# Kernel optimization log

Hardware: AMD Instinct MI355X
Metric: run time of the kernel (lower is better)

Reference implementation:

```python
import jax, jax.numpy as jnp
import numpy as np
import math

EPS = 1e-5
K = 4        # conv kernel size
N = 16       # d_state


def setup_inputs() -> dict:
    key = jax.random.key(0)
    b, l, d = 1, 2048, 1024
    di = 2 * d                      # inner channels after split
    dt_rank = math.ceil(d / 16)     # 64
    ks = jax.random.split(key, 8)
    s = 0.02
    return {
        "x": jax.random.normal(ks[0], (b, l, d), jnp.float32),
        "norm_scale": jnp.ones((d,), jnp.float32),
        "w_in": jax.random.normal(ks[1], (d, 4 * d), jnp.float32) * s,
        "conv_w": jax.random.normal(ks[2], (K, 1, di), jnp.float32) * 0.2,
        "conv_b": jnp.zeros((di,), jnp.float32),
        "A_log": jax.random.normal(ks[3], (di, N), jnp.float32) * 0.5,
        "D": jax.random.normal(ks[4], (di,), jnp.float32) * 0.1,
        "w_xproj": jax.random.normal(ks[5], (di, dt_rank + 2 * N), jnp.float32) * s,
        "w_dt": jax.random.normal(ks[6], (dt_rank, di), jnp.float32) * s,
        "b_dt": jnp.zeros((di,), jnp.float32),
        "w_out": jax.random.normal(ks[7], (di, d), jnp.float32) * s,
    }


def _causal_depthwise_conv(x, w, b):
    # x: (b,l,c), w: (K,1,c). Original pads (K-1,K-1) then slices [:, :l] == causal left-pad.
    c = x.shape[-1]
    y = jax.lax.conv_general_dilated(
        x, w, window_strides=(1,), padding=[(K - 1, 0)],
        dimension_numbers=("NWC", "WIO", "NWC"), feature_group_count=c)
    return y + b


def reference(x, norm_scale, w_in, conv_w, conv_b, A_log, D, w_xproj, w_dt, b_dt, w_out):
    dt_rank = w_dt.shape[0]
    # RMSNorm (mean=False, bias=False), scale only
    h = x * jax.lax.rsqrt(jnp.mean(x * x, axis=-1, keepdims=True) + EPS) * norm_scale
    h = h @ w_in                         # (b,l,4d)
    xs, res = jnp.split(h, 2, axis=-1)   # each (b,l,2d)
    res = jax.nn.silu(res)
    xs = jax.nn.silu(_causal_depthwise_conv(xs, conv_w, conv_b))
    proj = xs @ w_xproj                  # (b,l,dt_rank+2N)
    delta, B, C = jnp.split(proj, [dt_rank, dt_rank + N], axis=-1)
    delta = jax.nn.softplus(delta @ w_dt + b_dt)          # (b,l,c)
    A = -jnp.exp(A_log)                                   # (c,n)
    deltaA = jnp.exp(delta[..., None] * A)                # (b,l,c,n)
    deltaBx = (delta * xs)[..., None] * B[:, :, None, :]  # (b,l,c,n)

    def combine(e_i, e_j):
        a_i, b_i = e_i
        a_j, b_j = e_j
        return (a_i * a_j, a_j * b_i + b_j)

    _, ys = jax.lax.associative_scan(combine, (deltaA, deltaBx), axis=1)
    y = jnp.einsum("blcn,bln->blc", ys, C)
    out = (y + xs * D) * res
    return x + out @ w_out
```

## Files before the change

### kernel.cpp

```cpp
#include <hip/hip_runtime.h>

typedef short short8 __attribute__((ext_vector_type(8)));
typedef float floatx4 __attribute__((ext_vector_type(4)));
typedef unsigned int u32;

__device__ __forceinline__ float b2f(unsigned short u) {
    union { unsigned int i; float f; } v; v.i = ((unsigned int)u) << 16; return v.f;
}
__device__ __forceinline__ float hi2f(u32 p) {
    union { unsigned int i; float f; } v; v.i = p & 0xFFFF0000u; return v.f;
}
__device__ __forceinline__ float lo2f(u32 p) {
    union { unsigned int i; float f; } v; v.i = p << 16; return v.f;
}
__device__ __forceinline__ unsigned short f2b(float f) {
    union { unsigned int i; float f; } v; v.f = f;
    unsigned int r = v.i + 0x7FFFu + ((v.i >> 16) & 1u);
    return (unsigned short)(r >> 16);
}
__device__ __forceinline__ float ld(const void* p, size_t i, int f) {
    return f ? ((const float*)p)[i] : b2f(((const unsigned short*)p)[i]);
}
__device__ __forceinline__ int dtf(const void* scale) {
    return (((const unsigned short*)scale)[0] == 0x3F80u) ? 0 : 1;
}
__device__ __forceinline__ void gload16(const unsigned short* g, unsigned short* l) {
    __builtin_amdgcn_global_load_lds(
        (const __attribute__((address_space(1))) u32*)(const void*)g,
        (__attribute__((address_space(3))) u32*)(void*)l, 16, 0, 0);
}
template<int CTRL>
__device__ __forceinline__ float dpp_add(float y) {
    union { float f; int i; } u, r;
    u.f = y;
    r.i = __builtin_amdgcn_update_dpp(0, u.i, CTRL, 0xF, 0xF, true);
    return y + r.f;
}
#define LOG2E 1.44269504f

__global__ __launch_bounds__(256) void prep_kernel(
    const void* x, const void* scale, unsigned short* __restrict__ h,
    const void* w_in, unsigned short* __restrict__ wT,
    const void* w_out, unsigned short* __restrict__ woT)
{
    const int f = dtf(scale);
    const int b = blockIdx.x, tid = threadIdx.x;
    if (b < 2048) {
        const int t = b;
        float xv[4];
        float ss = 0.f;
        #pragma unroll
        for (int j = 0; j < 4; j++) {
            xv[j] = ld(x, (size_t)t * 1024 + j * 256 + tid, f);
            ss += xv[j] * xv[j];
        }
        #pragma unroll
        for (int o = 32; o > 0; o >>= 1) ss += __shfl_down(ss, o);
        __shared__ float sr[4];
        if ((tid & 63) == 0) sr[tid >> 6] = ss;
        __syncthreads();
        float r = rsqrtf((sr[0] + sr[1] + sr[2] + sr[3]) * (1.f / 1024.f) + 1e-5f);
        #pragma unroll
        for (int j = 0; j < 4; j++) {
            int i = j * 256 + tid;
            h[(size_t)t * 1024 + i] = f2b(xv[j] * r * ld(scale, i, f));
        }
    } else if (b < 3072) {
        __shared__ unsigned short tile[64][68];
        const int idx = b - 2048;
        const int n0 = (idx & 63) * 64, k0 = (idx >> 6) * 64;
        #pragma unroll
        for (int j = 0; j < 16; j++) {
            int ii = tid + 256 * j, r = ii >> 6, c = ii & 63;
            tile[r][c] = f2b(ld(w_in, (size_t)(k0 + r) * 4096 + n0 + c, f));
        }
        __syncthreads();
        #pragma unroll
        for (int j = 0; j < 16; j++) {
            int ii = tid + 256 * j, r = ii >> 6, c = ii & 63;
            wT[(size_t)(n0 + r) * 1024 + k0 + c] = tile[c][r];
        }
    } else {
        __shared__ unsigned short tile[64][68];
        const int idx = b - 3072;
        const int n0 = (idx & 15) * 64, k0 = (idx >> 4) * 64;
        #pragma unroll
        for (int j = 0; j < 16; j++) {
            int ii = tid + 256 * j, r = ii >> 6, c = ii & 63;
            tile[r][c] = f2b(ld(w_out, (size_t)(k0 + r) * 1024 + n0 + c, f));
        }
        __syncthreads();
        #pragma unroll
        for (int j = 0; j < 16; j++) {
            int ii = tid + 256 * j, r = ii >> 6, c = ii & 63;
            woT[(size_t)(n0 + r) * 2048 + k0 + c] = tile[c][r];
        }
    }
}

template<int KDIM, int NDIM, int TM, int MODE>
__global__ __launch_bounds__(256) void gemm_bt_kernel(
    const unsigned short* __restrict__ A, const unsigned short* __restrict__ BT,
    void* out0, unsigned short* out1, const void* xres, const void* nscale)
{
    constexpr int RT = TM / 32;
    const int f = dtf(nscale);
    __shared__ __align__(16) unsigned short As[TM * 64];
    __shared__ __align__(16) unsigned short Bs[64 * 64];
    const int t = threadIdx.x, w = t >> 6, lane = t & 63;
    const int q = lane >> 4, low = lane & 15;
    const int row0 = blockIdx.y * TM, n0 = blockIdx.x * 64;
    const int wy = w >> 1, wx = w & 1;

    floatx4 acc[RT][2];
    #pragma unroll
    for (int i = 0; i < RT; i++)
        #pragma unroll
        for (int j = 0; j < 2; j++) acc[i][j] = (floatx4){0.f, 0.f, 0.f, 0.f};

    const int srow = lane >> 3, scol = (lane & 7) * 8;
    const unsigned short* a_src = A + (size_t)(row0 + w * (TM / 4) + srow) * KDIM + scol;
    const unsigned short* b_src = BT + (size_t)(n0 + w * 16 + srow) * KDIM + scol;

    for (int k0 = 0; k0 < KDIM; k0 += 64) {
        #pragma unroll
        for (int i = 0; i < TM / 32; i++)
            gload16(a_src + k0 + i * 8 * KDIM, &As[(w * (TM / 4) + i * 8) * 64]);
        #pragma unroll
        for (int i = 0; i < 2; i++)
            gload16(b_src + k0 + i * 8 * KDIM, &Bs[(w * 16 + i * 8) * 64]);
        __syncthreads();
        #pragma unroll
        for (int kh = 0; kh < 2; kh++) {
            short8 af[RT];
            #pragma unroll
            for (int rt = 0; rt < RT; rt++)
                af[rt] = *(const short8*)&As[(wy * (TM / 2) + rt * 16 + low) * 64 + kh * 32 + q * 8];
            #pragma unroll
            for (int nt = 0; nt < 2; nt++) {
                short8 bf = *(const short8*)&Bs[(wx * 32 + nt * 16 + low) * 64 + kh * 32 + q * 8];
                #pragma unroll
                for (int rt = 0; rt < RT; rt++)
                    acc[rt][nt] = __builtin_amdgcn_mfma_f32_16x16x32_bf16(af[rt], bf, acc[rt][nt], 0, 0, 0);
            }
        }
        __syncthreads();
    }

    #pragma unroll
    for (int nt = 0; nt < 2; nt++) {
        const int col = n0 + wx * 32 + nt * 16 + low;
        #pragma unroll
        for (int rt = 0; rt < RT; rt++) {
            #pragma unroll
            for (int r = 0; r < 4; r++) {
                const int row = row0 + wy * (TM / 2) + rt * 16 + q * 4 + r;
                float v = acc[rt][nt][r];
                if (MODE == 0) {
                    if (col < NDIM / 2) {
                        ((unsigned short*)out0)[(size_t)row * (NDIM / 2) + col] = f2b(v);
                    } else {
                        float s = v / (1.f + __expf(-v));
                        out1[(size_t)row * (NDIM / 2) + (col - NDIM / 2)] = f2b(s);
                    }
                } else {
                    size_t idx = (size_t)row * NDIM + col;
                    float o = v + ld(xres, idx, f);
                    if (f) ((float*)out0)[idx] = o;
                    else   ((unsigned short*)out0)[idx] = f2b(o);
                }
            }
        }
    }
}

__global__ __launch_bounds__(256) void conv_kernel(
    const unsigned short* __restrict__ xs_raw, const void* conv_w,
    const void* conv_b, unsigned short* __restrict__ xs_conv, const void* nscale)
{
    const int f = dtf(nscale);
    int id = blockIdx.x * 256 + threadIdx.x;
    int t = id >> 8, c8 = (id & 255) * 8;
    float acc[8];
    if (f) {
        const float* bf = (const float*)conv_b + c8;
        float4 b0 = *(const float4*)bf, b1 = *(const float4*)(bf + 4);
        acc[0] = b0.x; acc[1] = b0.y; acc[2] = b0.z; acc[3] = b0.w;
        acc[4] = b1.x; acc[5] = b1.y; acc[6] = b1.z; acc[7] = b1.w;
    } else {
        uint4 bv = *(const uint4*)((const unsigned short*)conv_b + c8);
        const unsigned short* bp = (const unsigned short*)&bv;
        #pragma unroll
        for (int j = 0; j < 8; j++) acc[j] = b2f(bp[j]);
    }
    #pragma unroll
    for (int k = 0; k < 4; k++) {
        int tt = t - 3 + k;
        if (tt >= 0) {
            uint4 xv = *(const uint4*)(xs_raw + (size_t)tt * 2048 + c8);
            const unsigned short* xp = (const unsigned short*)&xv;
            float wv[8];
            if (f) {
                const float* wf = (const float*)conv_w + (size_t)k * 2048 + c8;
                float4 w0 = *(const float4*)wf, w1 = *(const float4*)(wf + 4);
                wv[0] = w0.x; wv[1] = w0.y; wv[2] = w0.z; wv[3] = w0.w;
                wv[4] = w1.x; wv[5] = w1.y; wv[6] = w1.z; wv[7] = w1.w;
            } else {
                uint4 wu = *(const uint4*)((const unsigned short*)conv_w + (size_t)k * 2048 + c8);
                const unsigned short* wp = (const unsigned short*)&wu;
                #pragma unroll
                for (int j = 0; j < 8; j++) wv[j] = b2f(wp[j]);
            }
            #pragma unroll
            for (int j = 0; j < 8; j++) acc[j] += wv[j] * b2f(xp[j]);
        }
    }
    unsigned short outv[8];
    #pragma unroll
    for (int j = 0; j < 8; j++) {
        float s = acc[j] / (1.f + __expf(-acc[j]));
        outv[j] = f2b(s);
    }
    *(uint4*)(xs_conv + (size_t)t * 2048 + c8) = *(const uint4*)outv;
}

__global__ __launch_bounds__(256) void xproj_gemm_kernel(
    const unsigned short* __restrict__ A, const void* B,
    float* __restrict__ partials, const void* nscale)
{
    const int f = dtf(nscale);
    __shared__ __align__(16) unsigned short As[64 * 32];
    __shared__ __align__(16) unsigned short Bs[64 * 32];
    const int t = threadIdx.x;
    const int row0 = blockIdx.y * 64, n0 = blockIdx.x * 64;
    const int ks = blockIdx.z;
    const int wave = t >> 6, lane = t & 63;
    const int q = lane >> 4, low = lane & 15;
    floatx4 acc[4];
    #pragma unroll
    for (int i = 0; i < 4; i++) acc[i] = (floatx4){0.f, 0.f, 0.f, 0.f};
    const int ar = t >> 2, ac = (t & 3) * 8;
    const int bk = t >> 3, bn = (t & 7) * 8;
    const int col0 = n0 + bn;
    const int kbeg = ks * 256, kend = kbeg + 256;
    for (int k0 = kbeg; k0 < kend; k0 += 32) {
        uint4 av = *(const uint4*)(A + (size_t)(row0 + ar) * 2048 + k0 + ac);
        *(uint4*)&As[ar * 32 + ac] = av;
        unsigned short bu[8];
        if (col0 < 96) {
            if (f) {
                const float* Bf = (const float*)B + (size_t)(k0 + bk) * 96 + col0;
                float4 b0 = *(const float4*)Bf, b1 = *(const float4*)(Bf + 4);
                bu[0] = f2b(b0.x); bu[1] = f2b(b0.y); bu[2] = f2b(b0.z); bu[3] = f2b(b0.w);
                bu[4] = f2b(b1.x); bu[5] = f2b(b1.y); bu[6] = f2b(b1.z); bu[7] = f2b(b1.w);
            } else {
                uint4 bv = *(const uint4*)((const unsigned short*)B + (size_t)(k0 + bk) * 96 + col0);
                *(uint4*)bu = bv;
            }
        } else {
            #pragma unroll
            for (int j = 0; j < 8; j++) bu[j] = 0;
        }
        #pragma unroll
        for (int j = 0; j < 8; j++) Bs[(bn + j) * 32 + bk] = bu[j];
        __syncthreads();
        short8 af = *(const short8*)&As[(wave * 16 + low) * 32 + q * 8];
        #pragma unroll
        for (int i = 0; i < 4; i++) {
            short8 bfr = *(const short8*)&Bs[(i * 16 + low) * 32 + q * 8];
            acc[i] = __builtin_amdgcn_mfma_f32_16x16x32_bf16(af, bfr, acc[i], 0, 0, 0);
        }
        __syncthreads();
    }
    float* out = partials + (size_t)ks * (2048 * 128);
    #pragma unroll
    for (int i = 0; i < 4; i++) {
        int col = n0 + i * 16 + low;
        #pragma unroll
        for (int r = 0; r < 4; r++) {
            int row = row0 + wave * 16 + q * 4 + r;
            out[(size_t)row * 128 + col] = acc[i][r];
        }
    }
}

__global__ __launch_bounds__(256) void xproj_reduce_kernel(
    const float* __restrict__ partials, float* __restrict__ proj)
{
    int id = blockIdx.x * 256 + threadIdx.x;
    float s = 0.f;
    #pragma unroll
    for (int k = 0; k < 8; k++) s += partials[(size_t)k * (2048 * 128) + id];
    proj[id] = s;
}

__global__ __launch_bounds__(256) void delta_gemm_kernel(
    const float* __restrict__ proj, const void* B, const void* b_dt,
    unsigned short* __restrict__ delta, const void* nscale)
{
    const int f = dtf(nscale);
    __shared__ __align__(16) unsigned short As[64 * 32];
    __shared__ __align__(16) unsigned short Bs[64 * 32];
    const int t = threadIdx.x;
    const int row0 = blockIdx.y * 64, n0 = blockIdx.x * 64;
    const int wave = t >> 6, lane = t & 63;
    const int q = lane >> 4, low = lane & 15;
    floatx4 acc[4];
    #pragma unroll
    for (int i = 0; i < 4; i++) acc[i] = (floatx4){0.f, 0.f, 0.f, 0.f};
    const int ar = t >> 2, ac = (t & 3) * 8;
    const int bk = t >> 3, bn = (t & 7) * 8;
    #pragma unroll
    for (int k0 = 0; k0 < 64; k0 += 32) {
        const float* Ap = proj + (size_t)(row0 + ar) * 128 + k0 + ac;
        float4 a0 = *(const float4*)Ap, a1 = *(const float4*)(Ap + 4);
        As[ar * 32 + ac + 0] = f2b(a0.x); As[ar * 32 + ac + 1] = f2b(a0.y);
        As[ar * 32 + ac + 2] = f2b(a0.z); As[ar * 32 + ac + 3] = f2b(a0.w);
        As[ar * 32 + ac + 4] = f2b(a1.x); As[ar * 32 + ac + 5] = f2b(a1.y);
        As[ar * 32 + ac + 6] = f2b(a1.z); As[ar * 32 + ac + 7] = f2b(a1.w);
        unsigned short bu[8];
        if (f) {
            const float* Bp = (const float*)B + (size_t)(k0 + bk) * 2048 + n0 + bn;
            float4 b0 = *(const float4*)Bp, b1 = *(const float4*)(Bp + 4);
            bu[0] = f2b(b0.x); bu[1] = f2b(b0.y); bu[2] = f2b(b0.z); bu[3] = f2b(b0.w);
            bu[4] = f2b(b1.x); bu[5] = f2b(b1.y); bu[6] = f2b(b1.z); bu[7] = f2b(b1.w);
        } else {
            uint4 bv = *(const uint4*)((const unsigned short*)B + (size_t)(k0 + bk) * 2048 + n0 + bn);
            const unsigned short* bp = (const unsigned short*)&bv;
            #pragma unroll
            for (int j = 0; j < 8; j++) bu[j] = bp[j];
        }
        #pragma unroll
        for (int j = 0; j < 8; j++) Bs[(bn + j) * 32 + bk] = bu[j];
        __syncthreads();
        short8 af = *(const short8*)&As[(wave * 16 + low) * 32 + q * 8];
        #pragma unroll
        for (int i = 0; i < 4; i++) {
            short8 bfr = *(const short8*)&Bs[(i * 16 + low) * 32 + q * 8];
            acc[i] = __builtin_amdgcn_mfma_f32_16x16x32_bf16(af, bfr, acc[i], 0, 0, 0);
        }
        __syncthreads();
    }
    #pragma unroll
    for (int i = 0; i < 4; i++) {
        int col = n0 + i * 16 + low;
        float bias = ld(b_dt, col, f);
        #pragma unroll
        for (int r = 0; r < 4; r++) {
            int row = row0 + wave * 16 + q * 4 + r;
            float v = acc[i][r] + bias;
            float sp = fmaxf(v, 0.f) + log1pf(__expf(-fabsf(v)));
            delta[(size_t)row * 2048 + col] = f2b(sp);
        }
    }
}

__global__ __launch_bounds__(256) void scanA_kernel(
    const unsigned short* __restrict__ delta, const unsigned short* __restrict__ xs,
    const float* __restrict__ proj, const void* A_log,
    float* __restrict__ Aprod, float* __restrict__ Send, const void* nscale)
{
    const int f = dtf(nscale);
    const int chunk = blockIdx.x, c0 = blockIdx.y * 16, t0 = chunk * 64;
    __shared__ __align__(16) u32 dxl[16 * 68];
    __shared__ __align__(16) float Bt[16 * 68];
    const int tid = threadIdx.x;
    #pragma unroll
    for (int j = 0; j < 2; j++) {
        int idx = tid + 256 * j;
        int t = idx >> 3, cp = (idx & 7) * 2;
        u32 dpair = *(const u32*)(delta + (size_t)(t0 + t) * 2048 + c0 + cp);
        u32 xpair = *(const u32*)(xs    + (size_t)(t0 + t) * 2048 + c0 + cp);
        dxl[cp * 68 + t]       = (dpair << 16) | (xpair & 0xFFFFu);
        dxl[(cp + 1) * 68 + t] = (dpair & 0xFFFF0000u) | (xpair >> 16);
    }
    #pragma unroll
    for (int j = 0; j < 4; j++) {
        int idx = tid + 256 * j;
        int t = idx >> 4, n = idx & 15;
        Bt[n * 68 + t] = proj[(size_t)(t0 + t) * 128 + 64 + n];
    }
    __syncthreads();
    const int cl = tid >> 4, n = tid & 15;
    const float A2 = -__expf(ld(A_log, (size_t)(c0 + cl) * 16 + n, f)) * LOG2E;
    float s = 0.f, dsum = 0.f;
    for (int t4 = 0; t4 < 64; t4 += 4) {
        uint4  dx4 = *(const uint4*)&dxl[cl * 68 + t4];
        float4 b4  = *(const float4*)&Bt[n * 68 + t4];
        const u32* dxp = (const u32*)&dx4;
        const float* bp = (const float*)&b4;
        #pragma unroll
        for (int j = 0; j < 4; j++) {
            u32 p = dxp[j];
            float dv = hi2f(p), xv = lo2f(p);
            float a = exp2f(dv * A2);
            s = a * s + dv * xv * bp[j];
            dsum += dv;
        }
    }
    size_t o = (size_t)chunk * 32768 + (size_t)c0 * 16 + tid;
    Aprod[o] = exp2f(A2 * dsum);
    Send[o]  = s;
}

__global__ __launch_bounds__(256) void scanB_kernel(
    const float* __restrict__ Aprod, const float* __restrict__ Send,
    float* __restrict__ prefix)
{
    int g = blockIdx.x * 256 + threadIdx.x;
    float a[32], b[32];
    #pragma unroll
    for (int k = 0; k < 32; k++) { a[k] = Aprod[(size_t)k * 32768 + g]; b[k] = Send[(size_t)k * 32768 + g]; }
    float s = 0.f;
    #pragma unroll
    for (int k = 0; k < 32; k++) { prefix[(size_t)k * 32768 + g] = s; s = a[k] * s + b[k]; }
}

__global__ __launch_bounds__(256) void scanC_kernel(
    const unsigned short* __restrict__ delta, const unsigned short* __restrict__ xs,
    const float* __restrict__ proj, const void* A_log, const void* Dv,
    const float* __restrict__ prefix,
    const unsigned short* __restrict__ res, unsigned short* __restrict__ inner,
    const void* nscale)
{
    const int f = dtf(nscale);
    const int chunk = blockIdx.x, c0 = blockIdx.y * 16, t0 = chunk * 64;
    __shared__ __align__(16) u32 dxl[16 * 68];
    __shared__ __align__(16) float Bt[16 * 68];
    __shared__ __align__(16) float Ct[16 * 68];
    __shared__ __align__(16) float yl[16 * 68];
    __shared__ float Dl[16];
    const int tid = threadIdx.x;
    if (tid < 16) Dl[tid] = ld(Dv, c0 + tid, f);
    float s = prefix[(size_t)chunk * 32768 + (size_t)c0 * 16 + tid];
    #pragma unroll
    for (int j = 0; j < 2; j++) {
        int idx = tid + 256 * j;
        int t = idx >> 3, cp = (idx & 7) * 2;
        u32 dpair = *(const u32*)(delta + (size_t)(t0 + t) * 2048 + c0 + cp);
        u32 xpair = *(const u32*)(xs    + (size_t)(t0 + t) * 2048 + c0 + cp);
        dxl[cp * 68 + t]       = (dpair << 16) | (xpair & 0xFFFFu);
        dxl[(cp + 1) * 68 + t] = (dpair & 0xFFFF0000u) | (xpair >> 16);
    }
    #pragma unroll
    for (int j = 0; j < 4; j++) {
        int idx = tid + 256 * j;
        int t = idx >> 4, n = idx & 15;
        Bt[n * 68 + t] = proj[(size_t)(t0 + t) * 128 + 64 + n];
        Ct[n * 68 + t] = proj[(size_t)(t0 + t) * 128 + 80 + n];
    }
    __syncthreads();
    const int cl = tid >> 4, n = tid & 15;
    const float A2 = -__expf(ld(A_log, (size_t)(c0 + cl) * 16 + n, f)) * LOG2E;
    for (int t4 = 0; t4 < 64; t4 += 4) {
        uint4  dx4 = *(const uint4*)&dxl[cl * 68 + t4];
        float4 b4  = *(const float4*)&Bt[n * 68 + t4];
        float4 c4  = *(const float4*)&Ct[n * 68 + t4];
        const u32* dxp = (const u32*)&dx4;
        const float* bp = (const float*)&b4;
        const float* cp = (const float*)&c4;
        #pragma unroll
        for (int j = 0; j < 4; j++) {
            u32 p = dxp[j];
            float dv = hi2f(p), xv = lo2f(p);
            float a = exp2f(dv * A2);
            s = a * s + dv * xv * bp[j];
            float y = s * cp[j];
            y = dpp_add<0x111>(y);
            y = dpp_add<0x112>(y);
            y = dpp_add<0x114>(y);
            y = dpp_add<0x118>(y);
            if (n == 15) yl[cl * 68 + t4 + j] = y;
        }
    }
    __syncthreads();
    const int et = tid >> 2, ech = (tid & 3) * 4;
    size_t gbase = (size_t)(t0 + et) * 2048 + c0 + ech;
    uint2 rv2 = *(const uint2*)(res + gbase);
    const unsigned short* rp = (const unsigned short*)&rv2;
    unsigned short outv[4];
    #pragma unroll
    for (int j = 0; j < 4; j++) {
        int c = ech + j;
        float y  = yl[c * 68 + et];
        float xv = lo2f(dxl[c * 68 + et]);
        float o  = (y + xv * Dl[c]) * b2f(rp[j]);
        outv[j] = f2b(o);
    }
    *(uint2*)(inner + gbase) = *(const uint2*)outv;
}

extern "C" void kernel_launch(void* const* d_in, const int* in_sizes, int n_in,
                              void* d_out, int out_size, void* d_ws, size_t ws_size,
                              hipStream_t stream) {
    const void* x       = d_in[0];
    const void* nscale  = d_in[1];
    const void* w_in    = d_in[2];
    const void* conv_w  = d_in[3];
    const void* conv_b  = d_in[4];
    const void* A_log   = d_in[5];
    const void* Dv      = d_in[6];
    const void* w_xproj = d_in[7];
    const void* w_dt    = d_in[8];
    const void* b_dt    = d_in[9];
    const void* w_out   = d_in[10];

    char* ws = (char*)d_ws;
    const size_t MB = 1048576;
    unsigned short* xs_raw  = (unsigned short*)(ws);
    unsigned short* res_s   = (unsigned short*)(ws + 8 * MB);
    unsigned short* xs_conv = (unsigned short*)(ws + 16 * MB);
    unsigned short* delta   = (unsigned short*)(ws + 24 * MB);
    unsigned short* h_norm  = (unsigned short*)(ws + 32 * MB);
    unsigned short* wT      = (unsigned short*)(ws + 36 * MB);
    unsigned short* woT     = (unsigned short*)(ws + 44 * MB);
    float*          partials= (float*)(ws + 48 * MB);
    float*          proj    = (float*)(ws + 56 * MB);
    float*          Aprod   = (float*)(ws + 57 * MB);
    float*          Send    = (float*)(ws + 61 * MB);
    float*          prefix  = (float*)(ws + 65 * MB);
    unsigned short* inner   = res_s;

    prep_kernel<<<3584, 256, 0, stream>>>(x, nscale, h_norm, w_in, wT, w_out, woT);
    gemm_bt_kernel<1024, 4096, 128, 0><<<dim3(64, 16), 256, 0, stream>>>(
        h_norm, wT, xs_raw, res_s, nullptr, nscale);
    conv_kernel<<<2048, 256, 0, stream>>>(xs_raw, conv_w, conv_b, xs_conv, nscale);
    xproj_gemm_kernel<<<dim3(2, 32, 8), 256, 0, stream>>>(xs_conv, w_xproj, partials, nscale);
    xproj_reduce_kernel<<<1024, 256, 0, stream>>>(partials, proj);
    delta_gemm_kernel<<<dim3(32, 32), 256, 0, stream>>>(proj, w_dt, b_dt, delta, nscale);
    scanA_kernel<<<dim3(32, 128), 256, 0, stream>>>(delta, xs_conv, proj, A_log, Aprod, Send, nscale);
    scanB_kernel<<<128, 256, 0, stream>>>(Aprod, Send, prefix);
    scanC_kernel<<<dim3(32, 128), 256, 0, stream>>>(delta, xs_conv, proj, A_log, Dv, prefix, res_s, inner, nscale);
    gemm_bt_kernel<2048, 1024, 64, 1><<<dim3(16, 32), 256, 0, stream>>>(
        inner, woT, d_out, nullptr, x, nscale);
}
```

Measured before the change: 273.4 us.

## Fuse delta GEMM with chunk-local scan pass A

Merges the delta projection GEMM and the first scan pass into one kernel. Each block computes a 64x64 tile of softplus(delta), keeps it in shared memory and runs the chunk-local scan over its 64 channels directly, so scan pass A no longer re-reads delta from global memory and one launch disappears. The cost is fewer blocks for the scan work (1024 instead of 4096), with each thread looping over four channel groups serially, which lowers parallelism and raises shared memory use per block.

Measured after the change: 280.0 us. +2.4%, slower.

```diff
diff --git a/kernel.cpp b/kernel.cpp
--- a/kernel.cpp
+++ b/kernel.cpp
@@ -294,15 +294,21 @@
     proj[id] = s;
 }
 
-__global__ __launch_bounds__(256) void delta_gemm_kernel(
+__global__ __launch_bounds__(256) void delta_scanA_kernel(
     const float* __restrict__ proj, const void* B, const void* b_dt,
-    unsigned short* __restrict__ delta, const void* nscale)
+    const unsigned short* __restrict__ xs, const void* A_log,
+    unsigned short* __restrict__ delta,
+    float* __restrict__ Aprod, float* __restrict__ Send, const void* nscale)
 {
     const int f = dtf(nscale);
     __shared__ __align__(16) unsigned short As[64 * 32];
     __shared__ __align__(16) unsigned short Bs[64 * 32];
+    __shared__ __align__(8) unsigned short dl[64 * 68];
+    __shared__ __align__(8) unsigned short xl[64 * 68];
+    __shared__ __align__(16) float Bt[16 * 68];
     const int t = threadIdx.x;
-    const int row0 = blockIdx.y * 64, n0 = blockIdx.x * 64;
+    const int chunk = blockIdx.y;
+    const int row0 = chunk * 64, n0 = blockIdx.x * 64;
     const int wave = t >> 6, lane = t & 63;
     const int q = lane >> 4, low = lane & 15;
     floatx4 acc[4];
@@ -343,64 +349,60 @@
     }
     #pragma unroll
     for (int i = 0; i < 4; i++) {
-        int col = n0 + i * 16 + low;
-        float bias = ld(b_dt, col, f);
+        int cloc = i * 16 + low;
+        float bias = ld(b_dt, n0 + cloc, f);
         #pragma unroll
         for (int r = 0; r < 4; r++) {
-            int row = row0 + wave * 16 + q * 4 + r;
+            int row = wave * 16 + q * 4 + r;
             float v = acc[i][r] + bias;
             float sp = fmaxf(v, 0.f) + log1pf(__expf(-fabsf(v)));
-            delta[(size_t)row * 2048 + col] = f2b(sp);
-        }
-    }
-}
-
-__global__ __launch_bounds__(256) void scanA_kernel(
-    const unsigned short* __restrict__ delta, const unsigned short* __restrict__ xs,
-    const float* __restrict__ proj, const void* A_log,
-    float* __restrict__ Aprod, float* __restrict__ Send, const void* nscale)
-{
-    const int f = dtf(nscale);
-    const int chunk = blockIdx.x, c0 = blockIdx.y * 16, t0 = chunk * 64;
-    __shared__ __align__(16) u32 dxl[16 * 68];
-    __shared__ __align__(16) float Bt[16 * 68];
-    const int tid = threadIdx.x;
+            unsigned short us = f2b(sp);
+            delta[(size_t)(row0 + row) * 2048 + n0 + cloc] = us;
+            dl[cloc * 68 + row] = us;
+        }
+    }
     #pragma unroll
     for (int j = 0; j < 2; j++) {
-        int idx = tid + 256 * j;
-        int t = idx >> 3, cp = (idx & 7) * 2;
-        u32 dpair = *(const u32*)(delta + (size_t)(t0 + t) * 2048 + c0 + cp);
-        u32 xpair = *(const u32*)(xs    + (size_t)(t0 + t) * 2048 + c0 + cp);
-        dxl[cp * 68 + t]       = (dpair << 16) | (xpair & 0xFFFFu);
-        dxl[(cp + 1) * 68 + t] = (dpair & 0xFFFF0000u) | (xpair >> 16);
+        int idx = t + 256 * j;
+        int tt = idx >> 3, cp = (idx & 7) * 8;
+        uint4 xv = *(const uint4*)(xs + (size_t)(row0 + tt) * 2048 + n0 + cp);
+        const unsigned short* xp = (const unsigned short*)&xv;
+        #pragma unroll
+        for (int jj = 0; jj < 8; jj++) xl[(cp + jj) * 68 + tt] = xp[jj];
     }
     #pragma unroll
     for (int j = 0; j < 4; j++) {
-        int idx = tid + 256 * j;
-        int t = idx >> 4, n = idx & 15;
-        Bt[n * 68 + t] = proj[(size_t)(t0 + t) * 128 + 64 + n];
+        int idx = t + 256 * j;
+        int tt = idx >> 4, n = idx & 15;
+        Bt[n * 68 + tt] = proj[(size_t)(row0 + tt) * 128 + 64 + n];
     }
     __syncthreads();
-    const int cl = tid >> 4, n = tid & 15;
-    const float A2 = -__expf(ld(A_log, (size_t)(c0 + cl) * 16 + n, f)) * LOG2E;
-    float s = 0.f, dsum = 0.f;
-    for (int t4 = 0; t4 < 64; t4 += 4) {
-        uint4  dx4 = *(const uint4*)&dxl[cl * 68 + t4];
-        float4 b4  = *(const float4*)&Bt[n * 68 + t4];
-        const u32* dxp = (const u32*)&dx4;
-        const float* bp = (const float*)&b4;
-        #pragma unroll
-        for (int j = 0; j < 4; j++) {
-            u32 p = dxp[j];
-            float dv = hi2f(p), xv = lo2f(p);
-            float a = exp2f(dv * A2);
-            s = a * s + dv * xv * bp[j];
-            dsum += dv;
-        }
-    }
-    size_t o = (size_t)chunk * 32768 + (size_t)c0 * 16 + tid;
-    Aprod[o] = exp2f(A2 * dsum);
-    Send[o]  = s;
+    const int cl = t >> 4, n = t & 15;
+    #pragma unroll
+    for (int cg = 0; cg < 4; cg++) {
+        const int cloc = cg * 16 + cl;
+        const int cglob = n0 + cloc;
+        const float A2 = -__expf(ld(A_log, (size_t)cglob * 16 + n, f)) * LOG2E;
+        float s = 0.f, dsum = 0.f;
+        for (int t4 = 0; t4 < 64; t4 += 4) {
+            ushort4 d4 = *(const ushort4*)&dl[cloc * 68 + t4];
+            ushort4 x4 = *(const ushort4*)&xl[cloc * 68 + t4];
+            float4  b4 = *(const float4*)&Bt[n * 68 + t4];
+            const unsigned short* dp = (const unsigned short*)&d4;
+            const unsigned short* xp = (const unsigned short*)&x4;
+            const float* bp = (const float*)&b4;
+            #pragma unroll
+            for (int j = 0; j < 4; j++) {
+                float dv = b2f(dp[j]), xv = b2f(xp[j]);
+                float a = exp2f(dv * A2);
+                s = a * s + dv * xv * bp[j];
+                dsum += dv;
+            }
+        }
+        size_t o = (size_t)chunk * 32768 + (size_t)cglob * 16 + n;
+        Aprod[o] = exp2f(A2 * dsum);
+        Send[o]  = s;
+    }
 }
 
 __global__ __launch_bounds__(256) void scanB_kernel(
@@ -527,8 +529,8 @@
     conv_kernel<<<2048, 256, 0, stream>>>(xs_raw, conv_w, conv_b, xs_conv, nscale);
     xproj_gemm_kernel<<<dim3(2, 32, 8), 256, 0, stream>>>(xs_conv, w_xproj, partials, nscale);
     xproj_reduce_kernel<<<1024, 256, 0, stream>>>(partials, proj);
-    delta_gemm_kernel<<<dim3(32, 32), 256, 0, stream>>>(proj, w_dt, b_dt, delta, nscale);
-    scanA_kernel<<<dim3(32, 128), 256, 0, stream>>>(delta, xs_conv, proj, A_log, Aprod, Send, nscale);
+    delta_scanA_kernel<<<dim3(32, 32), 256, 0, stream>>>(
+        proj, w_dt, b_dt, xs_conv, A_log, delta, Aprod, Send, nscale);
     scanB_kernel<<<128, 256, 0, stream>>>(Aprod, Send, prefix);
     scanC_kernel<<<dim3(32, 128), 256, 0, stream>>>(delta, xs_conv, proj, A_log, Dv, prefix, res_s, inner, nscale);
     gemm_bt_kernel<2048, 1024, 64, 1><<<dim3(16, 32), 256, 0, stream>>>(
```
